# Performance work log

Hardware: AMD Instinct MI355X
Metric: run time of the kernel (lower is better)

Reference implementation:

```python
import jax, jax.numpy as jnp
import numpy as np
from jax import lax

NS, C_IN, C_FEAT, CROP = 16, 3, 32, 256


def _conv(x, w, b):
    # 3x3 stride-1 'SAME' conv == padding=1 in torch
    y = lax.conv_general_dilated(x, w, (1, 1), 'SAME',
                                 dimension_numbers=('NCHW', 'OIHW', 'NCHW'))
    return y + b[None, :, None, None]


def _lrn(x, size=5, alpha=1e-4, beta=0.75, k=1.0):
    # PyTorch LocalResponseNorm: x / (k + alpha/size * sum_window x^2)^beta
    pad = size // 2
    sq = jnp.pad(x * x, ((0, 0), (pad, pad), (0, 0), (0, 0)))
    c = x.shape[1]
    win = sum(sq[:, i:i + c] for i in range(size))
    return x / (k + (alpha / size) * win) ** beta


def setup_inputs() -> dict:
    key = jax.random.key(0)
    ks = jax.random.split(key, 6)
    s = 0.05
    h = np.hanning(CROP).astype(np.float32)
    cos_window = jnp.asarray(np.outer(h, h))
    return {
        'z': jax.random.normal(ks[0], (NS, C_IN, CROP, CROP), jnp.float32),
        'w1': jax.random.normal(ks[1], (C_FEAT, C_IN, 3, 3), jnp.float32) * s,
        'b1': jax.random.normal(ks[2], (C_FEAT,), jnp.float32) * s,
        'w2': jax.random.normal(ks[3], (C_FEAT, C_FEAT, 3, 3), jnp.float32) * s,
        'b2': jax.random.normal(ks[4], (C_FEAT,), jnp.float32) * s,
        'cos_window': cos_window,
        'wf': jax.random.normal(ks[5], (1, C_FEAT, CROP, CROP // 2 + 1, 2), jnp.float32) * s,
    }


def reference(z, w1, b1, w2, b2, cos_window, wf):
    # feature extractor: conv -> relu -> conv -> LRN
    f = jax.nn.relu(_conv(z, w1, b1))
    f = _lrn(_conv(f, w2, b2))
    f = f * cos_window  # (ns, 32, crop, crop)
    zf = jnp.fft.rfft2(f, axes=(-2, -1))  # (ns, 32, crop, crop//2+1) complex
    # faithful to source: w_star = conj(wf), and the loop always uses w_star[0, 1]
    # (fixed channel 1) multiplied with zf[c, l], accumulated over l. wf is detached.
    wc = lax.stop_gradient(wf[0, 1, :, :, 0] - 1j * wf[0, 1, :, :, 1])
    ftrans = wc[None, None] * jnp.sum(zf, axis=1, keepdims=True)  # (ns,1,crop,crop//2+1)
    response = jnp.fft.irfft2(ftrans, s=(CROP, CROP), axes=(-2, -1))
    return response  # (ns, 1, crop, crop)
```

## Files before the change

kernel.cpp:

```cpp
#include <hip/hip_runtime.h>
#include <math.h>

#define NS   16
#define CIN  3
#define CF   32
#define CROP 256
#define KH   129

typedef _Float16 half8  __attribute__((ext_vector_type(8)));
typedef _Float16 half4v __attribute__((ext_vector_type(4)));
typedef _Float16 half2v __attribute__((ext_vector_type(2)));
typedef float    f32x4  __attribute__((ext_vector_type(4)));
typedef unsigned int u32x4 __attribute__((ext_vector_type(4)));

__device__ __forceinline__ half8 neg8(half8 v) {
    u32x4 u = __builtin_bit_cast(u32x4, v);
    u ^= (u32x4){0x80008000u, 0x80008000u, 0x80008000u, 0x80008000u};
    return __builtin_bit_cast(half8, u);
}

#define X_OFF 0
#define Z_OFF 21504
#define LDS_BYTES 23904

__device__ __forceinline__ int xaddr(int q, int s) {
    return X_OFF + (q << 6) + ((s ^ ((q >> 1) & 3)) << 4);
}

__device__ __forceinline__ int pi_of(int co) {
    int h = co >> 3, j = co & 7;
    return (j < 4) ? (h * 4 + j) : (16 + h * 4 + j - 4);
}
__device__ __forceinline__ int cinv_of(int p) {
    int h = (p & 15) >> 2;
    int j = (p & 3) + ((p >= 16) ? 4 : 0);
    return h * 8 + j;
}

__device__ __forceinline__ void split_pair(float v0, float v1,
                                           half2v* hp, half2v* lp) {
    _Float16 h0 = (_Float16)v0, h1 = (_Float16)v1;
    *hp = (half2v){h0, h1};
    *lp = (half2v){(_Float16)(v0 - (float)h0), (_Float16)(v1 - (float)h1)};
}

__global__ __launch_bounds__(256)
void prep(const float* __restrict__ w1, const float* __restrict__ w2,
          _Float16* __restrict__ w1pk, _Float16* __restrict__ w2lin,
          _Float16* __restrict__ TAh, _Float16* __restrict__ TAl,
          _Float16* __restrict__ G1h, _Float16* __restrict__ G1l,
          _Float16* __restrict__ G3h, _Float16* __restrict__ G3l,
          _Float16* __restrict__ TCh, _Float16* __restrict__ TCl)
{
    const int bid = blockIdx.x, tid = threadIdx.x;

    if (bid >= 67) {
        int base = (bid - 67) * 4096;
        #pragma unroll
        for (int i = 0; i < 16; ++i) {
            int e = base + tid + i * 256;
            if (e < 9216) {
                int co = e / 288;
                int r  = e - co * 288;
                int ci = r / 9, k9 = r - ci * 9;
                w2lin[(k9 * 32 + pi_of(co)) * 32 + ci] = (_Float16)w2[e];
            } else if (e < 9344) {
                int t = e - 9216;
                int lane = t & 63;
                int p = (t >> 6) * 16 + (lane & 15);
                int c = cinv_of(p);
                #pragma unroll
                for (int j = 0; j < 8; ++j) {
                    int k = ((lane >> 4) << 3) + j;
                    w1pk[t * 8 + j] = (k < 27) ? (_Float16)w1[c * 27 + k]
                                               : (_Float16)0.f;
                }
            }
        }
        return;
    }

    __shared__ float cs[256], sn[256];
    {
        float s, c;
        sincosf(0.02454369260617025967f * (float)tid, &s, &c);
        cs[tid] = c; sn[tid] = s;
    }
    __syncthreads();

    if (bid < 17) {
        int base = bid * 2048 + tid;
        #pragma unroll
        for (int i = 0; i < 8; ++i) {
            int p = base + i * 256;
            int j0 = (p & 3) * 2, lane = (p >> 2) & 63, q = p >> 8;
            int nt = q % 17, ks = q / 17;
            int x0 = ks * 32 + ((lane >> 4) << 3) + j0;
            int c = nt * 16 + (lane & 15);
            float v0 = 0.f, v1 = 0.f;
            if (c <= 128) {
                v0 =  cs[(x0 * c) & 255];
                v1 =  cs[((x0 + 1) * c) & 255];
            } else if (c >= 136 && c <= 264) {
                int cc = c - 136;
                v0 = -sn[(x0 * cc) & 255];
                v1 = -sn[((x0 + 1) * cc) & 255];
            }
            half2v hv, lv; split_pair(v0, v1, &hv, &lv);
            ((half2v*)TAh)[p] = hv; ((half2v*)TAl)[p] = lv;
        }
    } else if (bid < 49) {
        int base = (bid - 17) * 2048 + tid;
        #pragma unroll
        for (int i = 0; i < 8; ++i) {
            int p = base + i * 256;
            int j0 = (p & 3) * 2, lane = (p >> 2) & 63, q = p >> 8;
            int nt = q & 15, ks = q >> 4;
            int kk0 = ks * 32 + ((lane >> 4) << 3) + j0;
            int m  = nt * 16 + (lane & 15);
            int part = kk0 >> 8;
            int y0 = kk0 & 255;
            int i0 = (y0 * m) & 255, i1 = ((y0 + 1) * m) & 255;
            float cv0 = cs[i0], s0 = sn[i0], cv1 = cs[i1], s1 = sn[i1];
            half2v hv, lv;
            float a0 = part ? s0 : cv0,  a1 = part ? s1 : cv1;
            split_pair(a0, a1, &hv, &lv);
            ((half2v*)G1h)[p] = hv; ((half2v*)G1l)[p] = lv;
            a0 = (part ? -s0 : cv0) * (1.f/256.f);
            a1 = (part ? -s1 : cv1) * (1.f/256.f);
            split_pair(a0, a1, &hv, &lv);
            ((half2v*)G3h)[p] = hv; ((half2v*)G3l)[p] = lv;
        }
    } else {
        int base = (bid - 49) * 2048 + tid;
        #pragma unroll
        for (int i = 0; i < 8; ++i) {
            int p = base + i * 256;
            int j0 = (p & 3) * 2, lane = (p >> 2) & 63, q = p >> 8;
            int nt = q & 15, ks = q >> 4;
            int kk0 = ks * 32 + ((lane >> 4) << 3) + j0;
            int x  = nt * 16 + (lane & 15);
            int part = (kk0 >= 144) ? 1 : 0;
            int k0 = kk0 - part * 144;
            float v0 = 0.f, v1 = 0.f;
            if (k0 <= 128) {
                float w0 = (k0 == 0 || k0 == 128) ? 1.f : 2.f;
                int ii = (k0 * x) & 255;
                v0 = (part ? -w0 * sn[ii] : w0 * cs[ii]) * (1.f/256.f);
            }
            int k1 = k0 + 1;
            if (k1 <= 128) {
                float w1w = (k1 == 0 || k1 == 128) ? 1.f : 2.f;
                int ii = (k1 * x) & 255;
                v1 = (part ? -w1w * sn[ii] : w1w * cs[ii]) * (1.f/256.f);
            }
            half2v hv, lv; split_pair(v0, v1, &hv, &lv);
            ((half2v*)TCh)[p] = hv; ((half2v*)TCl)[p] = lv;
        }
    }
}

__global__ __launch_bounds__(256, 5)
void fused_features(const float* __restrict__ z,
                    const _Float16* __restrict__ w1pk,
                    const float* __restrict__ b1,
                    const _Float16* __restrict__ w2lin,
                    const float* __restrict__ b2,
                    const float* __restrict__ cosw,
                    _Float16* __restrict__ g2h, _Float16* __restrict__ g2l)
{
    __shared__ __align__(16) unsigned char smem[LDS_BYTES];
    _Float16* ztile = (_Float16*)(smem + Z_OFF);

    const int tid  = threadIdx.x;
    const int lane = tid & 63;
    const int wv   = tid >> 6;
    const int l15  = lane & 15;
    const int lhi  = lane >> 4;

    const int n  = blockIdx.z;
    const int bx = blockIdx.x, by = blockIdx.y;
    const int fy0 = by * 16 - 1;
    const int fx0 = bx * 16 - 1;

    const int zy0 = by * 16 - 2;
    const int zx0 = bx * 16 - 2;
    for (int idx = tid; idx < CIN * 400; idx += 256) {
        int ci = idx / 400;
        int r  = idx - ci * 400;
        int yy = r / 20, xx = r - yy * 20;
        int gy = zy0 + yy, gx = zx0 + xx;
        float v = 0.0f;
        if ((unsigned)gy < CROP && (unsigned)gx < CROP)
            v = z[((n * CIN + ci) * CROP + gy) * CROP + gx];
        ztile[idx] = (_Float16)v;
    }

    half8 w1f0 = *(const half8*)(w1pk + lane * 8);
    half8 w1f1 = *(const half8*)(w1pk + 512 + lane * 8);
    float bias1v[2][4], bias2v[2][4];
    #pragma unroll
    for (int cg = 0; cg < 2; ++cg)
        #pragma unroll
        for (int r = 0; r < 4; ++r) {
            bias1v[cg][r] = b1[8 * lhi + 4 * cg + r];
            bias2v[cg][r] = b2[8 * lhi + 4 * cg + r];
        }

    int offs[8];
    #pragma unroll
    for (int j = 0; j < 8; ++j) {
        int k = lhi * 8 + j;
        int ci = k / 9, rr = k - ci * 9;
        int ky = rr / 3, kx = rr - ky * 3;
        offs[j] = (k < 27) ? (ci * 400 + ky * 20 + kx) : 0;
    }
    __syncthreads();

    const f32x4 zero4 = {0.f, 0.f, 0.f, 0.f};
    for (int t = wv; t < 21; t += 4) {
        int qp = t * 16 + l15;
        int qpc = qp < 324 ? qp : 323;
        int y = qpc / 18, x = qpc - y * 18;
        const _Float16* zb = ztile + y * 20 + x;
        half8 bfrag;
        #pragma unroll
        for (int j = 0; j < 8; ++j) bfrag[j] = zb[offs[j]];
        f32x4 d0 = __builtin_amdgcn_mfma_f32_16x16x32_f16(w1f0, bfrag, zero4, 0, 0, 0);
        f32x4 d1 = __builtin_amdgcn_mfma_f32_16x16x32_f16(w1f1, bfrag, zero4, 0, 0, 0);
        int gy = fy0 + y, gx = fx0 + x;
        bool ok = ((unsigned)gy < CROP) && ((unsigned)gx < CROP) && (qp < 324);
        half8 o8;
        #pragma unroll
        for (int r = 0; r < 4; ++r) {
            float v0 = ok ? fmaxf(d0[r] + bias1v[0][r], 0.f) : 0.f;
            float v1 = ok ? fmaxf(d1[r] + bias1v[1][r], 0.f) : 0.f;
            o8[r]     = (_Float16)v0;
            o8[4 + r] = (_Float16)v1;
        }
        *(half8*)(smem + xaddr(qp, lhi)) = o8;
    }
    __syncthreads();

    f32x4 acc[4][2];
    #pragma unroll
    for (int tt = 0; tt < 4; ++tt)
        #pragma unroll
        for (int cg = 0; cg < 2; ++cg)
            #pragma unroll
            for (int r = 0; r < 4; ++r)
                acc[tt][cg][r] = bias2v[cg][r];

    #pragma unroll
    for (int k9 = 0; k9 < 9; ++k9) {
        const int ky = k9 / 3, kx = k9 - 3 * ky;
        half8 af0 = *(const half8*)(w2lin + (k9 * 32 + l15)      * 32 + lhi * 8);
        half8 af1 = *(const half8*)(w2lin + (k9 * 32 + l15 + 16) * 32 + lhi * 8);
        #pragma unroll
        for (int tt = 0; tt < 4; ++tt) {
            int q = (wv * 4 + tt + ky) * 18 + l15 + kx;
            half8 bf = *(const half8*)(smem + xaddr(q, lhi));
            acc[tt][0] = __builtin_amdgcn_mfma_f32_16x16x32_f16(af0, bf, acc[tt][0], 0, 0, 0);
            acc[tt][1] = __builtin_amdgcn_mfma_f32_16x16x32_f16(af1, bf, acc[tt][1], 0, 0, 0);
        }
    }

    const bool bot = (lhi == 0), top = (lhi == 3);
    #pragma unroll
    for (int tt = 0; tt < 4; ++tt) {
        float aA0 = acc[tt][0][0], aA1 = acc[tt][0][1],
              aA2 = acc[tt][0][2], aA3 = acc[tt][0][3];
        float aB0 = acc[tt][1][0], aB1 = acc[tt][1][1],
              aB2 = acc[tt][1][2], aB3 = acc[tt][1][3];
        float sA0 = aA0 * aA0, sA1 = aA1 * aA1, sA2 = aA2 * aA2, sA3 = aA3 * aA3;
        float sB0 = aB0 * aB0, sB1 = aB1 * aB1, sB2 = aB2 * aB2, sB3 = aB3 * aB3;
        int up = (lane + 16) & 63, dn = (lane + 48) & 63;
        float em2 = __shfl(sB2, dn); em2 = bot ? 0.f : em2;
        float em1 = __shfl(sB3, dn); em1 = bot ? 0.f : em1;
        float ep8 = __shfl(sA0, up); ep8 = top ? 0.f : ep8;
        float ep9 = __shfl(sA1, up); ep9 = top ? 0.f : ep9;
        float s = 0.f, win = em2 + em1 + sA0 + sA1 + sA2;
        float t2, f;
        t2 = 2e-5f * win; f = fmaf(t2, fmaf(t2, 0.65625f, -0.75f), 1.0f);
        s = fmaf(aA0, f, s);  win += sA3 - em2;
        t2 = 2e-5f * win; f = fmaf(t2, fmaf(t2, 0.65625f, -0.75f), 1.0f);
        s = fmaf(aA1, f, s);  win += sB0 - em1;
        t2 = 2e-5f * win; f = fmaf(t2, fmaf(t2, 0.65625f, -0.75f), 1.0f);
        s = fmaf(aA2, f, s);  win += sB1 - sA0;
        t2 = 2e-5f * win; f = fmaf(t2, fmaf(t2, 0.65625f, -0.75f), 1.0f);
        s = fmaf(aA3, f, s);  win += sB2 - sA1;
        t2 = 2e-5f * win; f = fmaf(t2, fmaf(t2, 0.65625f, -0.75f), 1.0f);
        s = fmaf(aB0, f, s);  win += sB3 - sA2;
        t2 = 2e-5f * win; f = fmaf(t2, fmaf(t2, 0.65625f, -0.75f), 1.0f);
        s = fmaf(aB1, f, s);  win += ep8 - sA3;
        t2 = 2e-5f * win; f = fmaf(t2, fmaf(t2, 0.65625f, -0.75f), 1.0f);
        s = fmaf(aB2, f, s);  win += ep9 - sB0;
        t2 = 2e-5f * win; f = fmaf(t2, fmaf(t2, 0.65625f, -0.75f), 1.0f);
        s = fmaf(aB3, f, s);
        s += __shfl_xor(s, 16);
        s += __shfl_xor(s, 32);
        if (lhi == 0) {
            int gy = by * 16 + wv * 4 + tt, gx = bx * 16 + l15;
            float val = s * cosw[gy * CROP + gx];
            _Float16 h = (_Float16)val;
            int o = (n * CROP + gy) * CROP + gx;
            g2h[o] = h;
            g2l[o] = (_Float16)(val - (float)h);
        }
    }
}

__global__ __launch_bounds__(256, 4)
void fft_rows(const _Float16* __restrict__ g2h, const _Float16* __restrict__ g2l,
              const _Float16* __restrict__ TAh, const _Float16* __restrict__ TAl,
              _Float16* __restrict__ Zth, _Float16* __restrict__ Ztl)
{
    const int lane = threadIdx.x & 63;
    const int wu = blockIdx.x * 4 + (threadIdx.x >> 6);
    const int mt = wu / 17, nt = wu - mt * 17;
    const int l15 = lane & 15, lhi = lane >> 4;
    const int rowA = mt * 16 + l15;

    f32x4 a0 = {}, a1 = {}, a2 = {};
    #pragma unroll
    for (int ks = 0; ks < 8; ++ks) {
        const int ao = rowA * 256 + ks * 32 + lhi * 8;
        half8 Ah = *(const half8*)(g2h + ao);
        half8 Al = *(const half8*)(g2l + ao);
        const int bo = ((ks * 17 + nt) * 64 + lane) * 8;
        half8 Bh = *(const half8*)(TAh + bo);
        half8 Bl = *(const half8*)(TAl + bo);
        a0 = __builtin_amdgcn_mfma_f32_16x16x32_f16(Ah, Bh, a0, 0, 0, 0);
        a1 = __builtin_amdgcn_mfma_f32_16x16x32_f16(Ah, Bl, a1, 0, 0, 0);
        a2 = __builtin_amdgcn_mfma_f32_16x16x32_f16(Al, Bh, a2, 0, 0, 0);
    }
    f32x4 acc;
    #pragma unroll
    for (int r = 0; r < 4; ++r) acc[r] = a0[r] + a1[r] + a2[r];

    const int rowD = mt * 16 + lhi * 4;
    const int n = rowD >> 8, y = rowD & 255;
    int c = nt * 16 + l15;
    int row_k = -1, koff = 0;
    if (c <= 128)                  { row_k = c;       koff = 0;   }
    else if (c >= 136 && c <= 264) { row_k = c - 136; koff = 256; }
    if (row_k >= 0) {
        half4v hv, lv;
        #pragma unroll
        for (int r = 0; r < 4; ++r) {
            float v = acc[r];
            _Float16 h = (_Float16)v;
            hv[r] = h; lv[r] = (_Float16)(v - (float)h);
        }
        size_t o = (size_t)(n * 144 + row_k) * 512 + koff + y;
        *(half4v*)(Zth + o) = hv;
        *(half4v*)(Ztl + o) = lv;
    }
}

__global__ __launch_bounds__(256, 2)
void fft_cols_mul(const _Float16* __restrict__ Zth, const _Float16* __restrict__ Ztl,
                  const _Float16* __restrict__ G1h, const _Float16* __restrict__ G1l,
                  const float* __restrict__ wf,
                  _Float16* __restrict__ Ph, _Float16* __restrict__ Pl)
{
    const int lane = threadIdx.x & 63;
    const int wu = blockIdx.x * 4 + (threadIdx.x >> 6);
    const int mt = wu >> 4, nt = wu & 15;
    const int l15 = lane & 15, lhi = lane >> 4;
    const int rowA = mt * 16 + l15;

    f32x4 r0 = {}, r1 = {}, r2 = {}, i0 = {}, i1 = {}, i2 = {};
    #pragma unroll
    for (int ks = 0; ks < 8; ++ks) {
        const int ao0 = rowA * 512 + ks * 32 + lhi * 8;
        half8 Ah0 = *(const half8*)(Zth + ao0);
        half8 Al0 = *(const half8*)(Ztl + ao0);
        half8 Ah1 = *(const half8*)(Zth + ao0 + 256);
        half8 Al1 = *(const half8*)(Ztl + ao0 + 256);
        const int bo0 = ((ks * 16 + nt) * 64 + lane) * 8;
        half8 B0h = *(const half8*)(G1h + bo0);
        half8 B0l = *(const half8*)(G1l + bo0);
        half8 B1h_ = *(const half8*)(G1h + bo0 + 65536);
        half8 B1l_ = *(const half8*)(G1l + bo0 + 65536);
        half8 nB1h = neg8(B1h_), nB1l = neg8(B1l_);
        r0 = __builtin_amdgcn_mfma_f32_16x16x32_f16(Ah0, B0h,  r0, 0, 0, 0);
        r1 = __builtin_amdgcn_mfma_f32_16x16x32_f16(Ah0, B0l,  r1, 0, 0, 0);
        r2 = __builtin_amdgcn_mfma_f32_16x16x32_f16(Al0, B0h,  r2, 0, 0, 0);
        r0 = __builtin_amdgcn_mfma_f32_16x16x32_f16(Ah1, B1h_, r0, 0, 0, 0);
        r1 = __builtin_amdgcn_mfma_f32_16x16x32_f16(Ah1, B1l_, r1, 0, 0, 0);
        r2 = __builtin_amdgcn_mfma_f32_16x16x32_f16(Al1, B1h_, r2, 0, 0, 0);
        i0 = __builtin_amdgcn_mfma_f32_16x16x32_f16(Ah0, nB1h, i0, 0, 0, 0);
        i1 = __builtin_amdgcn_mfma_f32_16x16x32_f16(Ah0, nB1l, i1, 0, 0, 0);
        i2 = __builtin_amdgcn_mfma_f32_16x16x32_f16(Al0, nB1h, i2, 0, 0, 0);
        i0 = __builtin_amdgcn_mfma_f32_16x16x32_f16(Ah1, B0h,  i0, 0, 0, 0);
        i1 = __builtin_amdgcn_mfma_f32_16x16x32_f16(Ah1, B0l,  i1, 0, 0, 0);
        i2 = __builtin_amdgcn_mfma_f32_16x16x32_f16(Al1, B0h,  i2, 0, 0, 0);
    }
    const int kbase = (mt % 9) * 16 + lhi * 4;
    const int rowP0 = mt * 16 + lhi * 4;
    const int m = nt * 16 + l15;
    const float* wf1 = wf + 256 * 129 * 2;
    #pragma unroll
    for (int r = 0; r < 4; ++r) {
        int k = kbase + r;
        float wr = wf1[(m * 129 + k) * 2 + 0];
        float wi = wf1[(m * 129 + k) * 2 + 1];
        float fr = r0[r] + r1[r] + r2[r];
        float fi = i0[r] + i1[r] + i2[r];
        float pr = wr * fr + wi * fi;
        float pi = wr * fi - wi * fr;
        size_t o = (size_t)(rowP0 + r) * 512 + m;
        _Float16 h;
        h = (_Float16)pr; Ph[o] = h;       Pl[o] = (_Float16)(pr - (float)h);
        h = (_Float16)pi; Ph[o + 256] = h; Pl[o + 256] = (_Float16)(pi - (float)h);
    }
}

__global__ __launch_bounds__(256, 2)
void fft_cols_inv(const _Float16* __restrict__ Ph, const _Float16* __restrict__ Pl,
                  const _Float16* __restrict__ G3h, const _Float16* __restrict__ G3l,
                  _Float16* __restrict__ Bth, _Float16* __restrict__ Btl)
{
    const int lane = threadIdx.x & 63;
    const int wu = blockIdx.x * 4 + (threadIdx.x >> 6);
    const int mt = wu >> 4, nt = wu & 15;
    const int l15 = lane & 15, lhi = lane >> 4;
    const int rowA = mt * 16 + l15;

    f32x4 r0 = {}, r1 = {}, r2 = {}, i0 = {}, i1 = {}, i2 = {};
    #pragma unroll
    for (int ks = 0; ks < 8; ++ks) {
        const int ao0 = rowA * 512 + ks * 32 + lhi * 8;
        half8 Ah0 = *(const half8*)(Ph + ao0);
        half8 Al0 = *(const half8*)(Pl + ao0);
        half8 Ah1 = *(const half8*)(Ph + ao0 + 256);
        half8 Al1 = *(const half8*)(Pl + ao0 + 256);
        const int bo0 = ((ks * 16 + nt) * 64 + lane) * 8;
        half8 B0h = *(const half8*)(G3h + bo0);
        half8 B0l = *(const half8*)(G3l + bo0);
        half8 B1h_ = *(const half8*)(G3h + bo0 + 65536);
        half8 B1l_ = *(const half8*)(G3l + bo0 + 65536);
        half8 nB1h = neg8(B1h_), nB1l = neg8(B1l_);
        r0 = __builtin_amdgcn_mfma_f32_16x16x32_f16(Ah0, B0h,  r0, 0, 0, 0);
        r1 = __builtin_amdgcn_mfma_f32_16x16x32_f16(Ah0, B0l,  r1, 0, 0, 0);
        r2 = __builtin_amdgcn_mfma_f32_16x16x32_f16(Al0, B0h,  r2, 0, 0, 0);
        r0 = __builtin_amdgcn_mfma_f32_16x16x32_f16(Ah1, B1h_, r0, 0, 0, 0);
        r1 = __builtin_amdgcn_mfma_f32_16x16x32_f16(Ah1, B1l_, r1, 0, 0, 0);
        r2 = __builtin_amdgcn_mfma_f32_16x16x32_f16(Al1, B1h_, r2, 0, 0, 0);
        i0 = __builtin_amdgcn_mfma_f32_16x16x32_f16(Ah0, nB1h, i0, 0, 0, 0);
        i1 = __builtin_amdgcn_mfma_f32_16x16x32_f16(Ah0, nB1l, i1, 0, 0, 0);
        i2 = __builtin_amdgcn_mfma_f32_16x16x32_f16(Al0, nB1h, i2, 0, 0, 0);
        i0 = __builtin_amdgcn_mfma_f32_16x16x32_f16(Ah1, B0h,  i0, 0, 0, 0);
        i1 = __builtin_amdgcn_mfma_f32_16x16x32_f16(Ah1, B0l,  i1, 0, 0, 0);
        i2 = __builtin_amdgcn_mfma_f32_16x16x32_f16(Al1, B0h,  i2, 0, 0, 0);
    }
    const int n = mt / 9;
    const int kbase = (mt % 9) * 16 + lhi * 4;
    const int y = nt * 16 + l15;
    size_t base = (size_t)(n * 256 + y) * 288 + kbase;
    half4v hv0, lv0, hv1, lv1;
    #pragma unroll
    for (int r = 0; r < 4; ++r) {
        float v = r0[r] + r1[r] + r2[r];
        _Float16 h = (_Float16)v;
        hv0[r] = h; lv0[r] = (_Float16)(v - (float)h);
        float v2 = i0[r] + i1[r] + i2[r];
        _Float16 h2 = (_Float16)v2;
        hv1[r] = h2; lv1[r] = (_Float16)(v2 - (float)h2);
    }
    *(half4v*)(Bth + base) = hv0;
    *(half4v*)(Btl + base) = lv0;
    *(half4v*)(Bth + base + 144) = hv1;
    *(half4v*)(Btl + base + 144) = lv1;
}

__global__ __launch_bounds__(256, 4)
void irfft_rows(const _Float16* __restrict__ Bth, const _Float16* __restrict__ Btl,
                const _Float16* __restrict__ TCh, const _Float16* __restrict__ TCl,
                float* __restrict__ out)
{
    const int lane = threadIdx.x & 63;
    const int wu = blockIdx.x * 4 + (threadIdx.x >> 6);
    const int mt = wu >> 4, nt = wu & 15;
    const int l15 = lane & 15, lhi = lane >> 4;
    const int rowA = mt * 16 + l15;

    f32x4 a0 = {}, a1 = {}, a2 = {};
    #pragma unroll
    for (int ks = 0; ks < 9; ++ks) {
        const int ao = rowA * 288 + ks * 32 + lhi * 8;
        half8 Ah = *(const half8*)(Bth + ao);
        half8 Al = *(const half8*)(Btl + ao);
        const int bo = ((ks * 16 + nt) * 64 + lane) * 8;
        half8 Bh = *(const half8*)(TCh + bo);
        half8 Bl = *(const half8*)(TCl + bo);
        a0 = __builtin_amdgcn_mfma_f32_16x16x32_f16(Ah, Bh, a0, 0, 0, 0);
        a1 = __builtin_amdgcn_mfma_f32_16x16x32_f16(Ah, Bl, a1, 0, 0, 0);
        a2 = __builtin_amdgcn_mfma_f32_16x16x32_f16(Al, Bh, a2, 0, 0, 0);
    }
    const int rowD = mt * 16 + lhi * 4;
    const int x = nt * 16 + l15;
    #pragma unroll
    for (int r = 0; r < 4; ++r)
        out[(size_t)(rowD + r) * 256 + x] = a0[r] + a1[r] + a2[r];
}

extern "C" void kernel_launch(void* const* d_in, const int* in_sizes, int n_in,
                              void* d_out, int out_size, void* d_ws, size_t ws_size,
                              hipStream_t stream)
{
    const float* z    = (const float*)d_in[0];
    const float* w1   = (const float*)d_in[1];
    const float* b1   = (const float*)d_in[2];
    const float* w2   = (const float*)d_in[3];
    const float* b2   = (const float*)d_in[4];
    const float* cosw = (const float*)d_in[5];
    const float* wf   = (const float*)d_in[6];
    float* out = (float*)d_out;

    char* p = (char*)d_ws;
    auto take = [&](size_t bytes) {
        char* r = p; p += (bytes + 255) & ~(size_t)255; return r;
    };
    _Float16* g2h = (_Float16*)take(4096 * 256 * 2);
    _Float16* g2l = (_Float16*)take(4096 * 256 * 2);
    _Float16* Zth = (_Float16*)take(2304 * 512 * 2);
    _Float16* Ztl = (_Float16*)take(2304 * 512 * 2);
    _Float16* Ph  = (_Float16*)take(2304 * 512 * 2);
    _Float16* Pl  = (_Float16*)take(2304 * 512 * 2);
    _Float16* TAh = (_Float16*)take(69632 * 2);
    _Float16* TAl = (_Float16*)take(69632 * 2);
    _Float16* G1h = (_Float16*)take(131072 * 2);
    _Float16* G1l = (_Float16*)take(131072 * 2);
    _Float16* G3h = (_Float16*)take(131072 * 2);
    _Float16* G3l = (_Float16*)take(131072 * 2);
    _Float16* TCh = (_Float16*)take(73728 * 2);
    _Float16* TCl = (_Float16*)take(73728 * 2);
    _Float16* w1pk  = (_Float16*)take(1024 * 2);
    _Float16* w2lin = (_Float16*)take(9216 * 2);
    _Float16* Bth = Zth;
    _Float16* Btl = Ztl;

    prep<<<70, 256, 0, stream>>>(w1, w2, w1pk, w2lin, TAh, TAl,
                                 G1h, G1l, G3h, G3l, TCh, TCl);
    fused_features<<<dim3(16, 16, NS), 256, 0, stream>>>(z, w1pk, b1, w2lin, b2,
                                                         cosw, g2h, g2l);
    fft_rows<<<1088, 256, 0, stream>>>(g2h, g2l, TAh, TAl, Zth, Ztl);
    fft_cols_mul<<<576, 256, 0, stream>>>(Zth, Ztl, G1h, G1l, wf, Ph, Pl);
    fft_cols_inv<<<576, 256, 0, stream>>>(Ph, Pl, G3h, G3l, Bth, Btl);
    irfft_rows<<<1024, 256, 0, stream>>>(Bth, Btl, TCh, TCl, out);
}
```

Measured before the change: 109.5 us.

## Pack frequency rows densely, add XCD-aware block swizzle, split prep wider

The intermediate spectrum is now stored with 129 rows per sample instead of a padded 144. This cuts the column-FFT grids from 576 to 516 blocks and drops the work done on padding rows. Block indices in the FFT kernels are remapped by an 8-way swizzle so neighbouring tiles share an XCD's L2. The prep kernel is spread across twice as many blocks. The output of the inverse column pass moves to its own buffer and is written as scalar half stores instead of vectorized half4 stores, which costs extra store instructions.

```diff
diff --git a/kernel.cpp b/kernel.cpp
--- a/kernel.cpp
+++ b/kernel.cpp
@@ -17,6 +17,12 @@
     u32x4 u = __builtin_bit_cast(u32x4, v);
     u ^= (u32x4){0x80008000u, 0x80008000u, 0x80008000u, 0x80008000u};
     return __builtin_bit_cast(half8, u);
+}
+
+__device__ __forceinline__ int swz8(int b, int nb) {
+    int q = nb >> 3, r = nb & 7;
+    int x = b & 7, o = b >> 3;
+    return (x < r ? x * (q + 1) : r * (q + 1) + (x - r) * q) + o;
 }
 
 #define X_OFF 0
@@ -54,8 +60,8 @@
 {
     const int bid = blockIdx.x, tid = threadIdx.x;
 
-    if (bid >= 67) {
-        int base = (bid - 67) * 4096;
+    if (bid >= 134) {
+        int base = (bid - 134) * 4096;
         #pragma unroll
         for (int i = 0; i < 16; ++i) {
             int e = base + tid + i * 256;
@@ -88,10 +94,10 @@
     }
     __syncthreads();
 
-    if (bid < 17) {
-        int base = bid * 2048 + tid;
-        #pragma unroll
-        for (int i = 0; i < 8; ++i) {
+    if (bid < 34) {
+        int base = bid * 1024 + tid;
+        #pragma unroll
+        for (int i = 0; i < 4; ++i) {
             int p = base + i * 256;
             int j0 = (p & 3) * 2, lane = (p >> 2) & 63, q = p >> 8;
             int nt = q % 17, ks = q / 17;
@@ -109,10 +115,10 @@
             half2v hv, lv; split_pair(v0, v1, &hv, &lv);
             ((half2v*)TAh)[p] = hv; ((half2v*)TAl)[p] = lv;
         }
-    } else if (bid < 49) {
-        int base = (bid - 17) * 2048 + tid;
-        #pragma unroll
-        for (int i = 0; i < 8; ++i) {
+    } else if (bid < 98) {
+        int base = (bid - 34) * 1024 + tid;
+        #pragma unroll
+        for (int i = 0; i < 4; ++i) {
             int p = base + i * 256;
             int j0 = (p & 3) * 2, lane = (p >> 2) & 63, q = p >> 8;
             int nt = q & 15, ks = q >> 4;
@@ -132,9 +138,9 @@
             ((half2v*)G3h)[p] = hv; ((half2v*)G3l)[p] = lv;
         }
     } else {
-        int base = (bid - 49) * 2048 + tid;
-        #pragma unroll
-        for (int i = 0; i < 8; ++i) {
+        int base = (bid - 98) * 1024 + tid;
+        #pragma unroll
+        for (int i = 0; i < 4; ++i) {
             int p = base + i * 256;
             int j0 = (p & 3) * 2, lane = (p >> 2) & 63, q = p >> 8;
             int nt = q & 15, ks = q >> 4;
@@ -316,7 +322,8 @@
               _Float16* __restrict__ Zth, _Float16* __restrict__ Ztl)
 {
     const int lane = threadIdx.x & 63;
-    const int wu = blockIdx.x * 4 + (threadIdx.x >> 6);
+    const int bsw = swz8(blockIdx.x, 1088);
+    const int wu = bsw * 4 + (threadIdx.x >> 6);
     const int mt = wu / 17, nt = wu - mt * 17;
     const int l15 = lane & 15, lhi = lane >> 4;
     const int rowA = mt * 16 + l15;
@@ -352,7 +359,7 @@
             _Float16 h = (_Float16)v;
             hv[r] = h; lv[r] = (_Float16)(v - (float)h);
         }
-        size_t o = (size_t)(n * 144 + row_k) * 512 + koff + y;
+        size_t o = (size_t)(n * 129 + row_k) * 512 + koff + y;
         *(half4v*)(Zth + o) = hv;
         *(half4v*)(Ztl + o) = lv;
     }
@@ -365,7 +372,8 @@
                   _Float16* __restrict__ Ph, _Float16* __restrict__ Pl)
 {
     const int lane = threadIdx.x & 63;
-    const int wu = blockIdx.x * 4 + (threadIdx.x >> 6);
+    const int bsw = swz8(blockIdx.x, 516);
+    const int wu = bsw * 4 + (threadIdx.x >> 6);
     const int mt = wu >> 4, nt = wu & 15;
     const int l15 = lane & 15, lhi = lane >> 4;
     const int rowA = mt * 16 + l15;
@@ -397,15 +405,15 @@
         i1 = __builtin_amdgcn_mfma_f32_16x16x32_f16(Ah1, B0l,  i1, 0, 0, 0);
         i2 = __builtin_amdgcn_mfma_f32_16x16x32_f16(Al1, B0h,  i2, 0, 0, 0);
     }
-    const int kbase = (mt % 9) * 16 + lhi * 4;
     const int rowP0 = mt * 16 + lhi * 4;
     const int m = nt * 16 + l15;
     const float* wf1 = wf + 256 * 129 * 2;
+    int n_ = rowP0 / 129;
+    int k_ = rowP0 - n_ * 129;
     #pragma unroll
     for (int r = 0; r < 4; ++r) {
-        int k = kbase + r;
-        float wr = wf1[(m * 129 + k) * 2 + 0];
-        float wi = wf1[(m * 129 + k) * 2 + 1];
+        float wr = wf1[(m * 129 + k_) * 2 + 0];
+        float wi = wf1[(m * 129 + k_) * 2 + 1];
         float fr = r0[r] + r1[r] + r2[r];
         float fi = i0[r] + i1[r] + i2[r];
         float pr = wr * fr + wi * fi;
@@ -414,6 +422,7 @@
         _Float16 h;
         h = (_Float16)pr; Ph[o] = h;       Pl[o] = (_Float16)(pr - (float)h);
         h = (_Float16)pi; Ph[o + 256] = h; Pl[o + 256] = (_Float16)(pi - (float)h);
+        if (++k_ == 129) { k_ = 0; ++n_; }
     }
 }
 
@@ -423,7 +432,8 @@
                   _Float16* __restrict__ Bth, _Float16* __restrict__ Btl)
 {
     const int lane = threadIdx.x & 63;
-    const int wu = blockIdx.x * 4 + (threadIdx.x >> 6);
+    const int bsw = swz8(blockIdx.x, 516);
+    const int wu = bsw * 4 + (threadIdx.x >> 6);
     const int mt = wu >> 4, nt = wu & 15;
     const int l15 = lane & 15, lhi = lane >> 4;
     const int rowA = mt * 16 + l15;
@@ -455,24 +465,21 @@
         i1 = __builtin_amdgcn_mfma_f32_16x16x32_f16(Ah1, B0l,  i1, 0, 0, 0);
         i2 = __builtin_amdgcn_mfma_f32_16x16x32_f16(Al1, B0h,  i2, 0, 0, 0);
     }
-    const int n = mt / 9;
-    const int kbase = (mt % 9) * 16 + lhi * 4;
+    const int rowP0 = mt * 16 + lhi * 4;
     const int y = nt * 16 + l15;
-    size_t base = (size_t)(n * 256 + y) * 288 + kbase;
-    half4v hv0, lv0, hv1, lv1;
+    int n_ = rowP0 / 129;
+    int k_ = rowP0 - n_ * 129;
     #pragma unroll
     for (int r = 0; r < 4; ++r) {
+        size_t base = (size_t)(n_ * 256 + y) * 288 + k_;
         float v = r0[r] + r1[r] + r2[r];
         _Float16 h = (_Float16)v;
-        hv0[r] = h; lv0[r] = (_Float16)(v - (float)h);
+        Bth[base] = h;  Btl[base] = (_Float16)(v - (float)h);
         float v2 = i0[r] + i1[r] + i2[r];
         _Float16 h2 = (_Float16)v2;
-        hv1[r] = h2; lv1[r] = (_Float16)(v2 - (float)h2);
-    }
-    *(half4v*)(Bth + base) = hv0;
-    *(half4v*)(Btl + base) = lv0;
-    *(half4v*)(Bth + base + 144) = hv1;
-    *(half4v*)(Btl + base + 144) = lv1;
+        Bth[base + 144] = h2;  Btl[base + 144] = (_Float16)(v2 - (float)h2);
+        if (++k_ == 129) { k_ = 0; ++n_; }
+    }
 }
 
 __global__ __launch_bounds__(256, 4)
@@ -481,7 +488,8 @@
                 float* __restrict__ out)
 {
     const int lane = threadIdx.x & 63;
-    const int wu = blockIdx.x * 4 + (threadIdx.x >> 6);
+    const int bsw = swz8(blockIdx.x, 1024);
+    const int wu = bsw * 4 + (threadIdx.x >> 6);
     const int mt = wu >> 4, nt = wu & 15;
     const int l15 = lane & 15, lhi = lane >> 4;
     const int rowA = mt * 16 + l15;
@@ -525,10 +533,12 @@
     };
     _Float16* g2h = (_Float16*)take(4096 * 256 * 2);
     _Float16* g2l = (_Float16*)take(4096 * 256 * 2);
-    _Float16* Zth = (_Float16*)take(2304 * 512 * 2);
-    _Float16* Ztl = (_Float16*)take(2304 * 512 * 2);
-    _Float16* Ph  = (_Float16*)take(2304 * 512 * 2);
-    _Float16* Pl  = (_Float16*)take(2304 * 512 * 2);
+    _Float16* Zth = (_Float16*)take(2064 * 512 * 2);
+    _Float16* Ztl = (_Float16*)take(2064 * 512 * 2);
+    _Float16* Ph  = (_Float16*)take(2064 * 512 * 2);
+    _Float16* Pl  = (_Float16*)take(2064 * 512 * 2);
+    _Float16* Bth = (_Float16*)take(4096 * 288 * 2);
+    _Float16* Btl = (_Float16*)take(4096 * 288 * 2);
     _Float16* TAh = (_Float16*)take(69632 * 2);
     _Float16* TAl = (_Float16*)take(69632 * 2);
     _Float16* G1h = (_Float16*)take(131072 * 2);
@@ -539,15 +549,13 @@
     _Float16* TCl = (_Float16*)take(73728 * 2);
     _Float16* w1pk  = (_Float16*)take(1024 * 2);
     _Float16* w2lin = (_Float16*)take(9216 * 2);
-    _Float16* Bth = Zth;
-    _Float16* Btl = Ztl;
-
-    prep<<<70, 256, 0, stream>>>(w1, w2, w1pk, w2lin, TAh, TAl,
-                                 G1h, G1l, G3h, G3l, TCh, TCl);
+
+    prep<<<137, 256, 0, stream>>>(w1, w2, w1pk, w2lin, TAh, TAl,
+                                  G1h, G1l, G3h, G3l, TCh, TCl);
     fused_features<<<dim3(16, 16, NS), 256, 0, stream>>>(z, w1pk, b1, w2lin, b2,
                                                          cosw, g2h, g2l);
     fft_rows<<<1088, 256, 0, stream>>>(g2h, g2l, TAh, TAl, Zth, Ztl);
-    fft_cols_mul<<<576, 256, 0, stream>>>(Zth, Ztl, G1h, G1l, wf, Ph, Pl);
-    fft_cols_inv<<<576, 256, 0, stream>>>(Ph, Pl, G3h, G3l, Bth, Btl);
+    fft_cols_mul<<<516, 256, 0, stream>>>(Zth, Ztl, G1h, G1l, wf, Ph, Pl);
+    fft_cols_inv<<<516, 256, 0, stream>>>(Ph, Pl, G3h, G3l, Bth, Btl);
     irfft_rows<<<1024, 256, 0, stream>>>(Bth, Btl, TCh, TCl, out);
 }
```

Result: no change. 110.6 us (+1.0%).
